# Performance work log

Hardware: AMD Instinct MI355X
Metric: run time of the kernel (lower is better)

The kernel has to match this reference:

```python
import jax, jax.numpy as jnp
import numpy as np
import math

N_HEADS = 16
D_EMBED = 1024
D_HEAD = D_EMBED // N_HEADS
SEQ_LEN = 4096
N_GRAPHS = 16


def setup_inputs() -> dict:
    key = jax.random.key(0)
    ks = jax.random.split(key, 6)
    x = jax.random.normal(ks[0], (SEQ_LEN, D_EMBED), dtype=jnp.float32)
    batch = jnp.sort(jax.random.randint(ks[1], (SEQ_LEN,), 0, N_GRAPHS, dtype=jnp.int64))
    s_in = 1.0 / math.sqrt(D_EMBED)
    W_in = jax.random.normal(ks[2], (D_EMBED, 3 * D_EMBED), dtype=jnp.float32) * s_in
    b_in = jnp.zeros((3 * D_EMBED,), dtype=jnp.float32)
    W_out = jax.random.normal(ks[3], (D_EMBED, D_EMBED), dtype=jnp.float32) * s_in
    b_out = jnp.zeros((D_EMBED,), dtype=jnp.float32)
    return {"x": x, "batch": batch, "W_in": W_in, "b_in": b_in, "W_out": W_out, "b_out": b_out}


def reference(x, batch, W_in, b_in, W_out, b_out):
    # x: [N, D]; batch: [N] graph ids
    n, d = x.shape
    qkv = x @ W_in + b_in                      # [N, 3D]
    q, k, v = jnp.split(qkv, 3, axis=-1)
    # [N, H, dh] -> [H, N, dh]
    q = q.reshape(n, N_HEADS, D_HEAD).transpose(1, 0, 2)
    k = k.reshape(n, N_HEADS, D_HEAD).transpose(1, 0, 2)
    v = v.reshape(n, N_HEADS, D_HEAD).transpose(1, 0, 2)
    weight = jnp.einsum('hnd,hmd->hnm', q, k)  # [H, N, N]
    # Faithful to original: in-block mask value is 1.0 (not 0), out-of-block -inf,
    # added BEFORE dividing by sqrt(d_head).
    same = batch[:, None] == batch[None, :]
    mask = jnp.where(same, 1.0, -jnp.inf).astype(weight.dtype)
    weight = (weight + mask) / math.sqrt(D_HEAD)
    weight = jax.nn.softmax(weight, axis=-1)
    out = jnp.einsum('hnm,hmd->hnd', weight, v)  # [H, N, dh]
    out = out.transpose(1, 0, 2).reshape(n, d)
    return out @ W_out + b_out
```

## Files before the change

### kernel.cpp

```cpp
#include <hip/hip_runtime.h>
#include <math.h>

#define NT 4096
#define DE 1024
#define NH 16
#define DH 64
#define NG 16

typedef unsigned short u16;
typedef __attribute__((ext_vector_type(8))) short short8;
typedef __attribute__((ext_vector_type(4))) float f32x4;

__device__ __forceinline__ u16 f2bf(float f) {
    unsigned u = __float_as_uint(f);
    unsigned r = (u + 0x7FFF + ((u >> 16) & 1)) >> 16;
    return (u16)r;
}
__device__ __forceinline__ u16 f2bf_trunc(float f) {
    return (u16)(__float_as_uint(f) >> 16);
}

__device__ __forceinline__ void gld_lds16(const u16* g, u16* l) {
    __builtin_amdgcn_global_load_lds(
        (const __attribute__((address_space(1))) unsigned int*)g,
        (__attribute__((address_space(3))) unsigned int*)l, 16, 0, 0);
}

__global__ __launch_bounds__(256) void prep_k(
        const float* __restrict__ x, u16* __restrict__ xb,
        const int* __restrict__ batch, int* __restrict__ bounds,
        const float* __restrict__ W_in, u16* __restrict__ Wt_in,
        const float* __restrict__ W_out, u16* __restrict__ Wt_out) {
    __shared__ float Ls[32][33];
    int bid = blockIdx.x;
    int t = threadIdx.x;
    if (bid < 4096) {
        if (bid == 0 && t <= NG) {
            int g = t, lo = 0, hi = NT;
            while (lo < hi) {
                int mid = (lo + hi) >> 1;
                if (batch[mid] < g) lo = mid + 1;
                else hi = mid;
            }
            bounds[g] = lo;
        }
        int i = bid * 256 + t;
        float4 v = *(const float4*)(x + (size_t)i * 4);
        ushort4 o = make_ushort4(f2bf(v.x), f2bf(v.y), f2bf(v.z), f2bf(v.w));
        *(ushort4*)(xb + (size_t)i * 4) = o;
        return;
    }
    int tb = bid - 4096;
    const float* W; u16* Wt; int N, k0, n0;
    if (tb < 3072) { W = W_in;  Wt = Wt_in;  N = 3 * DE; k0 = (tb & 31) * 32; n0 = (tb >> 5) * 32; }
    else { tb -= 3072; W = W_out; Wt = Wt_out; N = DE;   k0 = (tb & 31) * 32; n0 = (tb >> 5) * 32; }
    int row = t >> 3;
    int c4  = (t & 7) * 4;
    float4 v = *(const float4*)(W + (size_t)(k0 + row) * N + n0 + c4);
    Ls[row][c4 + 0] = v.x; Ls[row][c4 + 1] = v.y;
    Ls[row][c4 + 2] = v.z; Ls[row][c4 + 3] = v.w;
    __syncthreads();
    ushort4 o = make_ushort4(f2bf(Ls[c4 + 0][row]), f2bf(Ls[c4 + 1][row]),
                             f2bf(Ls[c4 + 2][row]), f2bf(Ls[c4 + 3][row]));
    *(ushort4*)(Wt + (size_t)(n0 + row) * DE + k0 + c4) = o;
}

template<int FM, int FN, typename OutT>
__global__ __launch_bounds__(256) void gemm_mfma_bt(
        const u16* __restrict__ A, const u16* __restrict__ Bt,
        const float* __restrict__ bias, OutT* __restrict__ C,
        int M, int N, int K) {
    __shared__ u16 As[32 * FM * 64];
    __shared__ u16 Bs[32 * FN * 64];
    const int tid  = threadIdx.x;
    const int wave = tid >> 6;
    const int lane = tid & 63;
    const int l15  = lane & 15;
    const int quad = lane >> 4;
    const int m0 = blockIdx.y * 32 * FM;
    const int n0 = blockIdx.x * 32 * FN;
    const int wm = (wave >> 1) * 16 * FM;
    const int wn = (wave & 1) * 16 * FN;

    f32x4 acc[FM][FN];
#pragma unroll
    for (int i = 0; i < FM; ++i)
#pragma unroll
        for (int j = 0; j < FN; ++j) acc[i][j] = (f32x4){0.f, 0.f, 0.f, 0.f};

    const int srow = lane >> 3;
    const int scol = ((lane & 7) ^ srow) * 8;
    const int xq   = l15 & 7;

    for (int k0 = 0; k0 < K; k0 += 64) {
#pragma unroll
        for (int s = wave; s < 4 * FM; s += 4)
            gld_lds16(A + (size_t)(m0 + s * 8 + srow) * K + k0 + scol, &As[s * 512]);
#pragma unroll
        for (int s = wave; s < 4 * FN; s += 4)
            gld_lds16(Bt + (size_t)(n0 + s * 8 + srow) * K + k0 + scol, &Bs[s * 512]);
        __syncthreads();

#pragma unroll
        for (int kh = 0; kh < 2; ++kh) {
            const int xb_ = 4 * kh + quad;
            short8 af[FM], bf[FN];
#pragma unroll
            for (int it = 0; it < FM; ++it)
                af[it] = *(const short8*)&As[(wm + 16 * it + l15) * 64 + ((xb_ ^ xq) * 8)];
#pragma unroll
            for (int jt = 0; jt < FN; ++jt)
                bf[jt] = *(const short8*)&Bs[(wn + 16 * jt + l15) * 64 + ((xb_ ^ xq) * 8)];
#pragma unroll
            for (int it = 0; it < FM; ++it)
#pragma unroll
                for (int jt = 0; jt < FN; ++jt)
                    acc[it][jt] = __builtin_amdgcn_mfma_f32_16x16x32_bf16(
                        af[it], bf[jt], acc[it][jt], 0, 0, 0);
        }
        __syncthreads();
    }

#pragma unroll
    for (int jt = 0; jt < FN; ++jt) {
        int col = n0 + wn + 16 * jt + l15;
        float bv = bias[col];
#pragma unroll
        for (int it = 0; it < FM; ++it) {
            int rbase = m0 + wm + 16 * it + quad * 4;
#pragma unroll
            for (int r = 0; r < 4; ++r) {
                float v = acc[it][jt][r] + bv;
                if constexpr (sizeof(OutT) == 2)
                    C[(size_t)(rbase + r) * N + col] = (OutT)f2bf(v);
                else
                    C[(size_t)(rbase + r) * N + col] = v;
            }
        }
    }
}

__global__ __launch_bounds__(256) void attn_mfma_k(
        const u16* __restrict__ qkv, const int* __restrict__ bounds,
        u16* __restrict__ out) {
    const int h  = blockIdx.x;
    const int g  = blockIdx.y;
    const int qt = blockIdx.z;
    const int s0 = bounds[g];
    const int s1 = bounds[g + 1];
    const int q0 = s0 + qt * 64;
    if (q0 >= s1) return;
    const int nq = min(64, s1 - q0);

    __shared__ u16 Ks[2][64 * 64];
    __shared__ u16 Vt[2][64][72];
    __shared__ u16 Ps[64][72];

    const int tid  = threadIdx.x;
    const int wave = tid >> 6;
    const int lane = tid & 63;
    const int l15  = lane & 15;
    const int quad = lane >> 4;

    short8 qf[2];
    {
        int qrow = wave * 16 + l15;
        uint4 a = {0, 0, 0, 0}, b = {0, 0, 0, 0};
        if (qrow < nq) {
            const u16* src = qkv + (size_t)(q0 + qrow) * 3072 + h * 64 + quad * 8;
            a = *(const uint4*)src;
            b = *(const uint4*)(src + 32);
        }
        qf[0] = *(short8*)&a;
        qf[1] = *(short8*)&b;
    }

    short8 onesf;
#pragma unroll
    for (int j = 0; j < 8; ++j) onesf[j] = (short)0x3F80;

    f32x4 o_acc[4];
    f32x4 l_acc = (f32x4){0.f, 0.f, 0.f, 0.f};
#pragma unroll
    for (int ct = 0; ct < 4; ++ct) o_acc[ct] = (f32x4){0.f, 0.f, 0.f, 0.f};

    const int nIter = (s1 - s0 + 63) >> 6;
    const int srow = lane >> 3;
    const int scol = ((lane & 7) ^ srow) * 8;

    auto stageK = [&](int it2, int buf) {
#pragma unroll
        for (int i = 0; i < 2; ++i) {
            int s = wave + 4 * i;
            gld_lds16(qkv + (size_t)(s0 + it2 * 64 + s * 8 + srow) * 3072 + 1024 + h * 64 + scol,
                      &Ks[buf][s * 512]);
        }
    };
    auto stageV = [&](int it2, int buf) {
        int r0 = 2 * (tid & 31);
        int c0 = (tid >> 5) * 8;
        const u16* src = qkv + (size_t)(s0 + it2 * 64 + r0) * 3072 + 2048 + h * 64 + c0;
        uint4 a = *(const uint4*)src;
        uint4 b = *(const uint4*)(src + 3072);
        const u16* pa = (const u16*)&a;
        const u16* pb = (const u16*)&b;
#pragma unroll
        for (int j = 0; j < 8; ++j) {
            unsigned w = (unsigned)pa[j] | ((unsigned)pb[j] << 16);
            *(unsigned*)&Vt[buf][c0 + j][r0] = w;
        }
    };

    stageK(0, 0);
    stageV(0, 0);
    __syncthreads();

    const float CEXP = 0.125f * 1.44269504f;
    const int xq = l15 & 7;

    for (int it = 0; it < nIter; ++it) {
        const int k0 = s0 + it * 64;
        const int buf = it & 1;
        if (it + 1 < nIter) { stageK(it + 1, buf ^ 1); stageV(it + 1, buf ^ 1); }

        f32x4 s[4];
#pragma unroll
        for (int ct = 0; ct < 4; ++ct) {
            int row = ct * 16 + l15;
            short8 kf0 = *(const short8*)&Ks[buf][row * 64 + ((quad ^ xq) * 8)];
            short8 kf1 = *(const short8*)&Ks[buf][row * 64 + (((4 + quad) ^ xq) * 8)];
            f32x4 acc = (f32x4){0.f, 0.f, 0.f, 0.f};
            acc = __builtin_amdgcn_mfma_f32_16x16x32_bf16(qf[0], kf0, acc, 0, 0, 0);
            acc = __builtin_amdgcn_mfma_f32_16x16x32_bf16(qf[1], kf1, acc, 0, 0, 0);
            s[ct] = acc;
        }

        if (k0 + 64 <= s1) {
#pragma unroll
            for (int ct = 0; ct < 4; ++ct)
#pragma unroll
                for (int r = 0; r < 4; ++r)
                    Ps[wave * 16 + quad * 4 + r][ct * 16 + l15] =
                        f2bf_trunc(exp2f(s[ct][r] * CEXP));
        } else {
#pragma unroll
            for (int ct = 0; ct < 4; ++ct) {
                bool valid = (k0 + ct * 16 + l15) < s1;
#pragma unroll
                for (int r = 0; r < 4; ++r)
                    Ps[wave * 16 + quad * 4 + r][ct * 16 + l15] =
                        valid ? f2bf_trunc(exp2f(s[ct][r] * CEXP)) : (u16)0;
            }
        }

        short8 pf0 = *(const short8*)&Ps[wave * 16 + l15][quad * 8];
        short8 pf1 = *(const short8*)&Ps[wave * 16 + l15][quad * 8 + 32];

        l_acc = __builtin_amdgcn_mfma_f32_16x16x32_bf16(pf0, onesf, l_acc, 0, 0, 0);
        l_acc = __builtin_amdgcn_mfma_f32_16x16x32_bf16(pf1, onesf, l_acc, 0, 0, 0);
#pragma unroll
        for (int ct = 0; ct < 4; ++ct) {
            short8 vf0 = *(const short8*)&Vt[buf][ct * 16 + l15][quad * 8];
            short8 vf1 = *(const short8*)&Vt[buf][ct * 16 + l15][quad * 8 + 32];
            o_acc[ct] = __builtin_amdgcn_mfma_f32_16x16x32_bf16(pf0, vf0, o_acc[ct], 0, 0, 0);
            o_acc[ct] = __builtin_amdgcn_mfma_f32_16x16x32_bf16(pf1, vf1, o_acc[ct], 0, 0, 0);
        }
        __syncthreads();
    }

#pragma unroll
    for (int r = 0; r < 4; ++r) {
        int row = wave * 16 + quad * 4 + r;
        if (row < nq) {
            float inv = 1.f / l_acc[r];
#pragma unroll
            for (int ct = 0; ct < 4; ++ct)
                out[(size_t)(q0 + row) * 1024 + h * 64 + ct * 16 + l15] =
                    f2bf(o_acc[ct][r] * inv);
        }
    }
}

extern "C" void kernel_launch(void* const* d_in, const int* in_sizes, int n_in,
                              void* d_out, int out_size, void* d_ws, size_t ws_size,
                              hipStream_t stream) {
    const float* x     = (const float*)d_in[0];
    const int*   batch = (const int*)d_in[1];
    const float* W_in  = (const float*)d_in[2];
    const float* b_in  = (const float*)d_in[3];
    const float* W_out = (const float*)d_in[4];
    const float* b_out = (const float*)d_in[5];
    float* out = (float*)d_out;

    u16* qkvb   = (u16*)d_ws;
    u16* attnb  = qkvb + (size_t)NT * 3 * DE;
    u16* xb     = attnb + (size_t)NT * DE;
    u16* Wt_in  = xb + (size_t)NT * DE;
    u16* Wt_out = Wt_in + (size_t)3 * DE * DE;
    int* bounds = (int*)(Wt_out + (size_t)DE * DE);

    prep_k<<<8192, 256, 0, stream>>>(x, xb, batch, bounds, W_in, Wt_in, W_out, Wt_out);

    gemm_mfma_bt<4, 4, u16><<<dim3(3 * DE / 128, NT / 128), 256, 0, stream>>>(
        xb, Wt_in, b_in, qkvb, NT, 3 * DE, DE);

    attn_mfma_k<<<dim3(NH, NG, 8), 256, 0, stream>>>(qkvb, bounds, attnb);

    gemm_mfma_bt<2, 4, float><<<dim3(DE / 128, NT / 64), 256, 0, stream>>>(
        attnb, Wt_out, b_out, out, NT, DE, DE);
}
```

Measured before the change: 155.4 us.

## Process two 64-row query subtiles per attention block to reuse staged K/V

Each attention block now covers 128 query rows as two 64-row subtiles. Every staged K and V tile in LDS feeds both subtiles, and the grid's query-tile dimension is halved to match. This halves the global K/V loads and V transposes per query, and halves the LDS staging and barriers. In exchange it doubles the accumulator registers and the serial work per block, and launches fewer blocks, which may hurt occupancy and load balance.

After: 152.0 us. 1.02x faster.

```diff
diff --git a/kernel.cpp b/kernel.cpp
--- a/kernel.cpp
+++ b/kernel.cpp
@@ -148,9 +148,9 @@
     const int qt = blockIdx.z;
     const int s0 = bounds[g];
     const int s1 = bounds[g + 1];
-    const int q0 = s0 + qt * 64;
+    const int q0 = s0 + qt * 128;
     if (q0 >= s1) return;
-    const int nq = min(64, s1 - q0);
+    const int nq = min(128, s1 - q0);
 
     __shared__ u16 Ks[2][64 * 64];
     __shared__ u16 Vt[2][64][72];
@@ -162,27 +162,32 @@
     const int l15  = lane & 15;
     const int quad = lane >> 4;
 
-    short8 qf[2];
-    {
-        int qrow = wave * 16 + l15;
+    short8 qf[2][2];
+#pragma unroll
+    for (int qs = 0; qs < 2; ++qs) {
+        int qrow = qs * 64 + wave * 16 + l15;
         uint4 a = {0, 0, 0, 0}, b = {0, 0, 0, 0};
         if (qrow < nq) {
             const u16* src = qkv + (size_t)(q0 + qrow) * 3072 + h * 64 + quad * 8;
             a = *(const uint4*)src;
             b = *(const uint4*)(src + 32);
         }
-        qf[0] = *(short8*)&a;
-        qf[1] = *(short8*)&b;
+        qf[qs][0] = *(short8*)&a;
+        qf[qs][1] = *(short8*)&b;
     }
 
     short8 onesf;
 #pragma unroll
     for (int j = 0; j < 8; ++j) onesf[j] = (short)0x3F80;
 
-    f32x4 o_acc[4];
-    f32x4 l_acc = (f32x4){0.f, 0.f, 0.f, 0.f};
-#pragma unroll
-    for (int ct = 0; ct < 4; ++ct) o_acc[ct] = (f32x4){0.f, 0.f, 0.f, 0.f};
+    f32x4 o_acc[2][4];
+    f32x4 l_acc[2];
+#pragma unroll
+    for (int qs = 0; qs < 2; ++qs) {
+        l_acc[qs] = (f32x4){0.f, 0.f, 0.f, 0.f};
+#pragma unroll
+        for (int ct = 0; ct < 4; ++ct) o_acc[qs][ct] = (f32x4){0.f, 0.f, 0.f, 0.f};
+    }
 
     const int nIter = (s1 - s0 + 63) >> 6;
     const int srow = lane >> 3;
@@ -223,62 +228,69 @@
         const int buf = it & 1;
         if (it + 1 < nIter) { stageK(it + 1, buf ^ 1); stageV(it + 1, buf ^ 1); }
 
-        f32x4 s[4];
-#pragma unroll
-        for (int ct = 0; ct < 4; ++ct) {
-            int row = ct * 16 + l15;
-            short8 kf0 = *(const short8*)&Ks[buf][row * 64 + ((quad ^ xq) * 8)];
-            short8 kf1 = *(const short8*)&Ks[buf][row * 64 + (((4 + quad) ^ xq) * 8)];
-            f32x4 acc = (f32x4){0.f, 0.f, 0.f, 0.f};
-            acc = __builtin_amdgcn_mfma_f32_16x16x32_bf16(qf[0], kf0, acc, 0, 0, 0);
-            acc = __builtin_amdgcn_mfma_f32_16x16x32_bf16(qf[1], kf1, acc, 0, 0, 0);
-            s[ct] = acc;
-        }
-
-        if (k0 + 64 <= s1) {
-#pragma unroll
-            for (int ct = 0; ct < 4; ++ct)
-#pragma unroll
-                for (int r = 0; r < 4; ++r)
-                    Ps[wave * 16 + quad * 4 + r][ct * 16 + l15] =
-                        f2bf_trunc(exp2f(s[ct][r] * CEXP));
-        } else {
+        const bool fullTile = (k0 + 64 <= s1);
+
+#pragma unroll
+        for (int qs = 0; qs < 2; ++qs) {
+            f32x4 s[4];
 #pragma unroll
             for (int ct = 0; ct < 4; ++ct) {
-                bool valid = (k0 + ct * 16 + l15) < s1;
-#pragma unroll
-                for (int r = 0; r < 4; ++r)
-                    Ps[wave * 16 + quad * 4 + r][ct * 16 + l15] =
-                        valid ? f2bf_trunc(exp2f(s[ct][r] * CEXP)) : (u16)0;
-            }
-        }
-
-        short8 pf0 = *(const short8*)&Ps[wave * 16 + l15][quad * 8];
-        short8 pf1 = *(const short8*)&Ps[wave * 16 + l15][quad * 8 + 32];
-
-        l_acc = __builtin_amdgcn_mfma_f32_16x16x32_bf16(pf0, onesf, l_acc, 0, 0, 0);
-        l_acc = __builtin_amdgcn_mfma_f32_16x16x32_bf16(pf1, onesf, l_acc, 0, 0, 0);
-#pragma unroll
-        for (int ct = 0; ct < 4; ++ct) {
-            short8 vf0 = *(const short8*)&Vt[buf][ct * 16 + l15][quad * 8];
-            short8 vf1 = *(const short8*)&Vt[buf][ct * 16 + l15][quad * 8 + 32];
-            o_acc[ct] = __builtin_amdgcn_mfma_f32_16x16x32_bf16(pf0, vf0, o_acc[ct], 0, 0, 0);
-            o_acc[ct] = __builtin_amdgcn_mfma_f32_16x16x32_bf16(pf1, vf1, o_acc[ct], 0, 0, 0);
+                int row = ct * 16 + l15;
+                short8 kf0 = *(const short8*)&Ks[buf][row * 64 + ((quad ^ xq) * 8)];
+                short8 kf1 = *(const short8*)&Ks[buf][row * 64 + (((4 + quad) ^ xq) * 8)];
+                f32x4 acc = (f32x4){0.f, 0.f, 0.f, 0.f};
+                acc = __builtin_amdgcn_mfma_f32_16x16x32_bf16(qf[qs][0], kf0, acc, 0, 0, 0);
+                acc = __builtin_amdgcn_mfma_f32_16x16x32_bf16(qf[qs][1], kf1, acc, 0, 0, 0);
+                s[ct] = acc;
+            }
+
+            if (fullTile) {
+#pragma unroll
+                for (int ct = 0; ct < 4; ++ct)
+#pragma unroll
+                    for (int r = 0; r < 4; ++r)
+                        Ps[wave * 16 + quad * 4 + r][ct * 16 + l15] =
+                            f2bf_trunc(exp2f(s[ct][r] * CEXP));
+            } else {
+#pragma unroll
+                for (int ct = 0; ct < 4; ++ct) {
+                    bool valid = (k0 + ct * 16 + l15) < s1;
+#pragma unroll
+                    for (int r = 0; r < 4; ++r)
+                        Ps[wave * 16 + quad * 4 + r][ct * 16 + l15] =
+                            valid ? f2bf_trunc(exp2f(s[ct][r] * CEXP)) : (u16)0;
+                }
+            }
+
+            short8 pf0 = *(const short8*)&Ps[wave * 16 + l15][quad * 8];
+            short8 pf1 = *(const short8*)&Ps[wave * 16 + l15][quad * 8 + 32];
+
+            l_acc[qs] = __builtin_amdgcn_mfma_f32_16x16x32_bf16(pf0, onesf, l_acc[qs], 0, 0, 0);
+            l_acc[qs] = __builtin_amdgcn_mfma_f32_16x16x32_bf16(pf1, onesf, l_acc[qs], 0, 0, 0);
+#pragma unroll
+            for (int ct = 0; ct < 4; ++ct) {
+                short8 vf0 = *(const short8*)&Vt[buf][ct * 16 + l15][quad * 8];
+                short8 vf1 = *(const short8*)&Vt[buf][ct * 16 + l15][quad * 8 + 32];
+                o_acc[qs][ct] = __builtin_amdgcn_mfma_f32_16x16x32_bf16(pf0, vf0, o_acc[qs][ct], 0, 0, 0);
+                o_acc[qs][ct] = __builtin_amdgcn_mfma_f32_16x16x32_bf16(pf1, vf1, o_acc[qs][ct], 0, 0, 0);
+            }
         }
         __syncthreads();
     }
 
 #pragma unroll
-    for (int r = 0; r < 4; ++r) {
-        int row = wave * 16 + quad * 4 + r;
-        if (row < nq) {
-            float inv = 1.f / l_acc[r];
-#pragma unroll
-            for (int ct = 0; ct < 4; ++ct)
-                out[(size_t)(q0 + row) * 1024 + h * 64 + ct * 16 + l15] =
-                    f2bf(o_acc[ct][r] * inv);
-        }
-    }
+    for (int qs = 0; qs < 2; ++qs)
+#pragma unroll
+        for (int r = 0; r < 4; ++r) {
+            int row = qs * 64 + wave * 16 + quad * 4 + r;
+            if (row < nq) {
+                float inv = 1.f / l_acc[qs][r];
+#pragma unroll
+                for (int ct = 0; ct < 4; ++ct)
+                    out[(size_t)(q0 + row) * 1024 + h * 64 + ct * 16 + l15] =
+                        f2bf(o_acc[qs][ct][r] * inv);
+            }
+        }
 }
 
 extern "C" void kernel_launch(void* const* d_in, const int* in_sizes, int n_in,
@@ -304,7 +316,7 @@
     gemm_mfma_bt<4, 4, u16><<<dim3(3 * DE / 128, NT / 128), 256, 0, stream>>>(
         xb, Wt_in, b_in, qkvb, NT, 3 * DE, DE);
 
-    attn_mfma_k<<<dim3(NH, NG, 8), 256, 0, stream>>>(qkvb, bounds, attnb);
+    attn_mfma_k<<<dim3(NH, NG, 4), 256, 0, stream>>>(qkvb, bounds, attnb);
 
     gemm_mfma_bt<2, 4, float><<<dim3(DE / 128, NT / 64), 256, 0, stream>>>(
         attnb, Wt_out, b_out, out, NT, DE, DE);
```
